# Kernel tuning notes

Hardware: AMD Instinct MI355X
Metric: run time of the kernel (lower is better)

Reference implementation:

```python
import jax, jax.numpy as jnp
import numpy as np

IMG = 32            # feature-map side == image_size
B, HC = 8, 3        # batch, hint channels
C, NH, L = 256, 8, 8  # model_channels, nhead, num_encoder_layers
DFF = 1025
HIN = IMG * 8       # hint resolution (three stride-2 convs => /8)
NEIGH = (7, 7)
CONV_SHAPES = [(16, HC), (16, 16), (32, 16), (32, 32), (96, 32), (96, 96), (256, 96), (C, 256)]
STRIDES = [1, 1, 2, 1, 2, 1, 2, 1]


def setup_inputs() -> dict:
    key = jax.random.key(0)
    ks = jax.random.split(key, 32)
    inp = {"hint": jax.random.normal(ks[0], (B, HC, HIN, HIN), jnp.float32)}
    for i, (co, ci) in enumerate(CONV_SHAPES):
        inp[f"conv_w{i}"] = jax.random.normal(ks[1 + i], (co, ci, 3, 3), jnp.float32) * 0.05
    base = 9
    def p(shape, j):
        return jax.random.normal(ks[base + j], (L,) + shape, jnp.float32) * 0.02
    inp["in_proj_w"] = p((3 * C, C), 0)
    inp["in_proj_b"] = p((3 * C,), 1)
    inp["out_w"] = p((C, C), 2)
    inp["out_b"] = p((C,), 3)
    inp["lin1_w"] = p((DFF, C), 4)
    inp["lin1_b"] = p((DFF,), 5)
    inp["lin2_w"] = p((C, DFF), 6)
    inp["lin2_b"] = p((C,), 7)
    inp["ln1_w"] = jnp.ones((L, C), jnp.float32)
    inp["ln1_b"] = jnp.zeros((L, C), jnp.float32)
    inp["ln2_w"] = jnp.ones((L, C), jnp.float32)
    inp["ln2_b"] = jnp.zeros((L, C), jnp.float32)
    return inp


def _conv(x, w, s):
    # torch Conv2d(k=3, padding=1, stride=s, bias=False)
    return jax.lax.conv_general_dilated(x, w, (s, s), [(1, 1), (1, 1)],
                                        dimension_numbers=("NCHW", "OIHW", "NCHW"))


def _sine_pos(h, w, c):
    # DETR/UniAD PositionEmbeddingSine (normalize=False, temperature=1e4) -> (h*w, c)
    npf = c // 2
    y = jnp.broadcast_to(jnp.arange(1, h + 1, dtype=jnp.float32)[:, None], (h, w))
    x = jnp.broadcast_to(jnp.arange(1, w + 1, dtype=jnp.float32)[None, :], (h, w))
    dim_t = 10000.0 ** (2.0 * (jnp.arange(npf, dtype=jnp.float32) // 2) / npf)
    px = x[..., None] / dim_t
    py = y[..., None] / dim_t
    px = jnp.stack([jnp.sin(px[..., 0::2]), jnp.cos(px[..., 1::2])], -1).reshape(h, w, npf)
    py = jnp.stack([jnp.sin(py[..., 0::2]), jnp.cos(py[..., 1::2])], -1).reshape(h, w, npf)
    return jnp.concatenate([py, px], -1).reshape(h * w, c)


def _neigh_mask(h, w, hm, wm):
    # vectorized version of generate_mask: 0 inside the hm x wm neighborhood, -inf outside
    ih = jnp.arange(h)
    iw = jnp.arange(w)
    dh = jnp.abs(ih[:, None] - ih[None, :]) <= hm // 2   # (h, h)
    dw = jnp.abs(iw[:, None] - iw[None, :]) <= wm // 2   # (w, w)
    allowed = (dh[:, None, :, None] & dw[None, :, None, :]).reshape(h * w, h * w)
    return jnp.where(allowed, 0.0, -1e9).astype(jnp.float32)


def _ln(x, g, b):
    mu = x.mean(-1, keepdims=True)
    v = ((x - mu) ** 2).mean(-1, keepdims=True)
    return (x - mu) / jnp.sqrt(v + 1e-5) * g + b


def _forward(hint, conv_ws, params):
    x = hint
    for i, (w, s) in enumerate(zip(conv_ws, STRIDES)):
        x = _conv(x, w, s)
        if i < len(conv_ws) - 1:
            x = jax.nn.silu(x)
    b, c, h, w = x.shape
    src = x.reshape(b, c, h * w).transpose(0, 2, 1)          # (B, N, C), N h-major
    pos = _sine_pos(h, w, c)[None]                           # (1, N, C)
    mask = _neigh_mask(h, w, *NEIGH)                         # (N, N)
    dh = c // NH
    scale = 1.0 / np.sqrt(dh).astype(np.float32)

    def layer(s, p):
        ipw, ipb, ow, ob, l1w, l1b, l2w, l2b, g1, b1, g2, b2 = p
        qk_in = s + pos
        q = (qk_in @ ipw[:c].T + ipb[:c]).reshape(b, -1, NH, dh)
        k = (qk_in @ ipw[c:2 * c].T + ipb[c:2 * c]).reshape(b, -1, NH, dh)
        v = (s @ ipw[2 * c:].T + ipb[2 * c:]).reshape(b, -1, NH, dh)
        sc = jnp.einsum('bnhd,bmhd->bhnm', q, k) * scale + mask
        a = jax.nn.softmax(sc, -1)
        ctx = jnp.einsum('bhnm,bmhd->bnhd', a, v).reshape(b, -1, c)
        s = _ln(s + ctx @ ow.T + ob, g1, b1)                 # post-norm
        ff = jax.nn.relu(s @ l1w.T + l1b) @ l2w.T + l2b      # dropout inactive (eval)
        return _ln(s + ff, g2, b2), None

    src, _ = jax.lax.scan(layer, src, params)
    return src.transpose(0, 2, 1).reshape(b, c, h, w)        # '(h w) b c -> b c h w'


def reference(hint, conv_w0, conv_w1, conv_w2, conv_w3, conv_w4, conv_w5, conv_w6, conv_w7,
              in_proj_w, in_proj_b, out_w, out_b, lin1_w, lin1_b, lin2_w, lin2_b,
              ln1_w, ln1_b, ln2_w, ln2_b):
    conv_ws = (conv_w0, conv_w1, conv_w2, conv_w3, conv_w4, conv_w5, conv_w6, conv_w7)
    params = (in_proj_w, in_proj_b, out_w, out_b, lin1_w, lin1_b, lin2_w, lin2_b,
              ln1_w, ln1_b, ln2_w, ln2_b)
    return _forward(hint, conv_ws, params)
```

## Files before the change

### kernel.cpp

```cpp
#include <hip/hip_runtime.h>
#include <hip/hip_bf16.h>


typedef __bf16 bf16x8 __attribute__((ext_vector_type(8)));
typedef float f32x4 __attribute__((ext_vector_type(4)));
typedef unsigned short us8v __attribute__((ext_vector_type(8)));

__device__ __forceinline__ unsigned short f2bf(float f) {
  unsigned int u = __float_as_uint(f);
  unsigned int r = (u + 0x7fffu + ((u >> 16) & 1u)) >> 16;
  return (unsigned short)r;
}
__device__ __forceinline__ float bf2f(unsigned short h) {
  return __uint_as_float(((unsigned int)h) << 16);
}

#define GLD16(src, dst)                                                        \
  __builtin_amdgcn_global_load_lds(                                            \
      (const __attribute__((address_space(1))) unsigned int*)(src),            \
      (__attribute__((address_space(3))) unsigned int*)(dst), 16, 0, 0)

template<int BM, int BN, int NT, int MODE, int LNF = 0, int KTC = 0>
__global__ __launch_bounds__(NT) void k_gemm(
    const unsigned short* __restrict__ A, int lda,
    const unsigned short* __restrict__ Bw, int ldb,
    const float* __restrict__ bias, const float* __restrict__ posadd,
    float* __restrict__ C, unsigned short* __restrict__ Cb, int ldc,
    int K, int Nstore, int act, int omode, long long zsB, long long zsC,
    const unsigned short* __restrict__ zpage, int Ci, int Hi, int stride, int lw,
    int divm, int divs, const float* __restrict__ lng, const float* __restrict__ lnb)
{
  constexpr int NW = NT / 64;
  constexpr int NWN = (NT == 512) ? 4 : ((BN >= 128) ? 2 : 1);
  constexpr int NWM = NW / NWN;
  constexpr int WM = BM / NWM, WN = BN / NWN;
  constexpr int MF = WM / 16, NF = WN / 16;
  constexpr int AIS = (BM * 8) / NT;
  constexpr int BIS = (BN * 8) / NT;
  __shared__ unsigned short lA[2][BM * 64];
  __shared__ unsigned short lB[2][BN * 64];
  __shared__ float red[2][32][2];
  int tid = threadIdx.x, lane = tid & 63, wid = tid >> 6;
  int bm = blockIdx.x * BM, bn = blockIdx.y * BN;
  const unsigned short* Bz = Bw + (size_t)blockIdx.z * zsB;

  int j = (lane & 7) ^ (lane >> 3);
  int e8 = (j & 3) << 3;
  int halfl = j >> 2;

  size_t arow[AIS], brow[BIS];
  int hb[AIS], wb[AIS];
  size_t ab[AIS];
#pragma unroll
  for (int i = 0; i < AIS; ++i) {
    int rr = (wid + i * NW) * 8 + (lane >> 3);
    if constexpr (MODE == 0) {
      arow[i] = (size_t)(bm + rr) * lda + (j << 3);
    } else {
      int pos = bm + rr;
      int b = pos >> (2 * lw);
      int rem = pos & ((1 << (2 * lw)) - 1);
      int ho = rem >> lw, wo = rem & ((1 << lw) - 1);
      hb[i] = ho * stride - 1;
      wb[i] = wo * stride - 1;
      ab[i] = (size_t)b * Hi * Hi * Ci;
    }
  }
#pragma unroll
  for (int i = 0; i < BIS; ++i)
    brow[i] = (size_t)(bn + (wid + i * NW) * 8 + (lane >> 3)) * ldb + (j << 3);

  auto stage = [&](int buf, int kt) {
    if constexpr (MODE == 1) {
      int s0 = kt * 2, s1 = s0 + 1;
      int t0 = (s0 * divm) >> divs, t1 = (s1 * divm) >> divs;
      int cipw = Ci >> 5;
      int cc0 = (s0 - t0 * cipw) << 5, cc1 = (s1 - t1 * cipw) << 5;
      int kh0 = (t0 * 171) >> 9, kw0 = t0 - kh0 * 3;
      int kh1 = (t1 * 171) >> 9, kw1 = t1 - kh1 * 3;
      int kh = halfl ? kh1 : kh0;
      int kw = halfl ? kw1 : kw0;
      int cco = halfl ? cc1 : cc0;
      bool tv = (halfl ? t1 : t0) < 9;
#pragma unroll
      for (int i = 0; i < AIS; ++i) {
        int hi = hb[i] + kh, wi = wb[i] + kw;
        const unsigned short* ap =
            (tv && (unsigned)hi < (unsigned)Hi && (unsigned)wi < (unsigned)Hi)
                ? (A + ab[i] + (size_t)(hi * Hi + wi) * Ci + cco + e8)
                : zpage;
        GLD16(ap, &lA[buf][(wid + i * NW) * 512]);
      }
    } else {
#pragma unroll
      for (int i = 0; i < AIS; ++i)
        GLD16(A + arow[i] + kt * 64, &lA[buf][(wid + i * NW) * 512]);
    }
#pragma unroll
    for (int i = 0; i < BIS; ++i)
      GLD16(Bz + brow[i] + kt * 64, &lB[buf][(wid + i * NW) * 512]);
  };

  f32x4 acc[MF][NF];
#pragma unroll
  for (int m = 0; m < MF; ++m)
#pragma unroll
    for (int n = 0; n < NF; ++n)
#pragma unroll
      for (int q = 0; q < 4; ++q) acc[m][n][q] = 0.f;

  int wn = wid % NWN, wm = wid / NWN;
  int r0 = wm * WM + (lane & 15);
  int c0 = wn * WN + (lane & 15);
  int sl0 = (((lane >> 4)) ^ (lane & 7)) << 3;
  int sl1 = (((lane >> 4) + 4) ^ (lane & 7)) << 3;
  const int nkt = (KTC > 0) ? KTC : (K >> 6);
  int cur = 0;
  stage(0, 0);
#pragma unroll
  for (int kt = 0; kt < nkt; ++kt) {
    if (kt + 1 < nkt) {
      stage(cur ^ 1, kt + 1);
      asm volatile("s_waitcnt vmcnt(%0)" : : "n"(AIS + BIS) : "memory");
    } else {
      asm volatile("s_waitcnt vmcnt(0)" : : : "memory");
    }
    __builtin_amdgcn_s_barrier();
    asm volatile("" ::: "memory");
    bf16x8 a0[MF], a1[MF], b0[NF], b1[NF];
#pragma unroll
    for (int m = 0; m < MF; ++m) {
      a0[m] = *(const bf16x8*)&lA[cur][(r0 + m * 16) * 64 + sl0];
      a1[m] = *(const bf16x8*)&lA[cur][(r0 + m * 16) * 64 + sl1];
    }
#pragma unroll
    for (int n = 0; n < NF; ++n) {
      b0[n] = *(const bf16x8*)&lB[cur][(c0 + n * 16) * 64 + sl0];
      b1[n] = *(const bf16x8*)&lB[cur][(c0 + n * 16) * 64 + sl1];
    }
#pragma unroll
    for (int m = 0; m < MF; ++m)
#pragma unroll
      for (int n = 0; n < NF; ++n)
        acc[m][n] = __builtin_amdgcn_mfma_f32_16x16x32_bf16(a0[m], b0[n], acc[m][n], 0, 0, 0);
#pragma unroll
    for (int m = 0; m < MF; ++m)
#pragma unroll
      for (int n = 0; n < NF; ++n)
        acc[m][n] = __builtin_amdgcn_mfma_f32_16x16x32_bf16(a1[m], b1[n], acc[m][n], 0, 0, 0);
    asm volatile("" ::: "memory");
    __builtin_amdgcn_s_barrier();
    cur ^= 1;
  }

  int colb = bn + wn * WN + (lane & 15);
  int rowb = bm + wm * WM + ((lane >> 4) << 2);

  if constexpr (LNF) {
    float x[NF][4];
    float sums[4] = {0.f, 0.f, 0.f, 0.f}, sqs[4] = {0.f, 0.f, 0.f, 0.f};
#pragma unroll
    for (int n = 0; n < NF; ++n) {
      int col = colb + n * 16;
      float bs = bias[col];
#pragma unroll
      for (int q = 0; q < 4; ++q) {
        int row = rowb + q;
        float v = acc[0][n][q] + bs + C[(size_t)row * 256 + col];
        x[n][q] = v;
        sums[q] += v;
        sqs[q] += v * v;
      }
    }
#pragma unroll
    for (int q = 0; q < 4; ++q) {
      sums[q] += __shfl_xor(sums[q], 1); sqs[q] += __shfl_xor(sqs[q], 1);
      sums[q] += __shfl_xor(sums[q], 2); sqs[q] += __shfl_xor(sqs[q], 2);
      sums[q] += __shfl_xor(sums[q], 4); sqs[q] += __shfl_xor(sqs[q], 4);
      sums[q] += __shfl_xor(sums[q], 8); sqs[q] += __shfl_xor(sqs[q], 8);
    }
    int rl = wm * 16 + ((lane >> 4) << 2);
    if ((lane & 15) == 0) {
#pragma unroll
      for (int q = 0; q < 4; ++q) {
        red[wn][rl + q][0] = sums[q];
        red[wn][rl + q][1] = sqs[q];
      }
    }
    __syncthreads();
#pragma unroll
    for (int q = 0; q < 4; ++q) {
      float ts = sums[q] + red[wn ^ 1][rl + q][0];
      float tq = sqs[q] + red[wn ^ 1][rl + q][1];
      float mu = ts * (1.f / 256.f);
      float var = tq * (1.f / 256.f) - mu * mu;
      float rs = rsqrtf(var + 1e-5f);
      int row = rowb + q;
#pragma unroll
      for (int n = 0; n < NF; ++n) {
        int col = colb + n * 16;
        float o = (x[n][q] - mu) * rs * lng[col] + lnb[col];
        C[(size_t)row * 256 + col] = o;
        Cb[(size_t)row * 256 + col] = f2bf(o);
      }
    }
    return;
  }

  float* Cz = C ? C + (size_t)blockIdx.z * zsC : nullptr;
  unsigned short* Cbz = Cb ? Cb + (size_t)blockIdx.z * zsC : nullptr;
#pragma unroll
  for (int n = 0; n < NF; ++n) {
    int col = colb + n * 16;
    if (col >= Nstore) continue;
    float bs = bias ? bias[col] : 0.f;
#pragma unroll
    for (int m = 0; m < MF; ++m) {
#pragma unroll
      for (int q = 0; q < 4; ++q) {
        int row = rowb + m * 16 + q;
        float v = acc[m][n][q] + bs;
        if (posadd && col < 512) v += posadd[((row & 1023) << 9) + col];
        if (act == 1) v = fmaxf(v, 0.f);
        else if (act == 2) v = v / (1.f + __expf(-v));
        size_t off = (size_t)row * ldc + col;
        if (omode == 0) Cz[off] = v;
        else if (omode == 1) Cbz[off] = f2bf(v);
        else { Cz[off] = v; Cbz[off] = f2bf(v); }
      }
    }
  }
}

template<int S>
__global__ __launch_bounds__(256) void k_conv_direct(
    const unsigned short* __restrict__ x, const unsigned short* __restrict__ wp,
    int ldw, unsigned short* __restrict__ y, int Hi, int Ho, int Wo, int lwt)
{
  constexpr int HR = 7 * S + 3;
  constexpr int HC = 15 * S + 3;
  constexpr int HP = HR * HC;
  __shared__ unsigned short xs[HP * 40];
  __shared__ unsigned short wsh[32 * 312];
  int tid = threadIdx.x, lane = tid & 63, wv = tid >> 6;
  int b = blockIdx.y;
  int tr = blockIdx.x >> lwt, tc = blockIdx.x & ((1 << lwt) - 1);
  int hi0 = tr * 8 * S - 1, wi0 = tc * 16 * S - 1;

  for (int u = tid; u < HP * 8; u += 256) {
    int pix = u >> 3, part = u & 7;
    int hr = pix / HC, hcc = pix - hr * HC;
    int hi = hi0 + hr, wi = wi0 + hcc;
    ushort4 v = {0, 0, 0, 0};
    if ((unsigned)hi < (unsigned)Hi && (unsigned)wi < (unsigned)Hi)
      v = *(const ushort4*)(x + ((size_t)(b * Hi + hi) * Hi + wi) * 32 + part * 4);
    *(ushort4*)(&xs[pix * 40 + part * 4]) = v;
  }
  for (int u = tid; u < 2304; u += 256) {
    int co = u / 72, kk = (u - co * 72) * 4;
    *(ushort4*)(&wsh[co * 312 + kk]) = *(const ushort4*)(wp + (size_t)co * ldw + kk);
  }
  __syncthreads();

  int cL = lane & 15, kq = (lane >> 4) << 3;
  f32x4 acc[2][2];
#pragma unroll
  for (int m = 0; m < 2; ++m)
#pragma unroll
    for (int n = 0; n < 2; ++n)
#pragma unroll
      for (int q = 0; q < 4; ++q) acc[m][n][q] = 0.f;

#pragma unroll
  for (int tap = 0; tap < 9; ++tap) {
    const int kh = tap / 3, kw = tap % 3;
    bf16x8 af[2], bfr[2];
#pragma unroll
    for (int m = 0; m < 2; ++m) {
      int hr = (wv * 2 + m) * S + kh;
      int hc = cL * S + kw;
      af[m] = *(const bf16x8*)&xs[(hr * HC + hc) * 40 + kq];
    }
#pragma unroll
    for (int n = 0; n < 2; ++n)
      bfr[n] = *(const bf16x8*)&wsh[(cL + n * 16) * 312 + tap * 32 + kq];
#pragma unroll
    for (int m = 0; m < 2; ++m)
#pragma unroll
      for (int n = 0; n < 2; ++n)
        acc[m][n] = __builtin_amdgcn_mfma_f32_16x16x32_bf16(af[m], bfr[n], acc[m][n], 0, 0, 0);
  }

  int wo0 = tc * 16 + ((lane >> 4) << 2);
#pragma unroll
  for (int m = 0; m < 2; ++m) {
    int ho = tr * 8 + wv * 2 + m;
#pragma unroll
    for (int n = 0; n < 2; ++n) {
      int co = cL + n * 16;
#pragma unroll
      for (int q = 0; q < 4; ++q) {
        float v = acc[m][n][q];
        v = v / (1.f + __expf(-v));
        y[((size_t)(b * Ho + ho) * Wo + wo0 + q) * 32 + co] = f2bf(v);
      }
    }
  }
}

__global__ __launch_bounds__(256) void k_im2col0(
    const float* __restrict__ x, unsigned short* __restrict__ dst, int row0, int total)
{
  for (int idx = blockIdx.x * 256 + threadIdx.x; idx < total; idx += gridDim.x * 256) {
    int r = idx >> 6, e = idx & 63;
    int pos = row0 + r;
    int b = pos >> 16, rem = pos & 65535, ho = rem >> 8, wo = rem & 255;
    unsigned short val = 0;
    if (e < 27) {
      int t9 = e / 3, ci = e - t9 * 3;
      int hi = ho + (t9 / 3) - 1, wi = wo + (t9 - (t9 / 3) * 3) - 1;
      if ((unsigned)hi < 256u && (unsigned)wi < 256u)
        val = f2bf(x[(((size_t)b * 3 + ci) << 16) + (hi << 8) + wi]);
    }
    dst[idx] = val;
  }
}

__global__ __launch_bounds__(256) void k_wperm(
    const float* __restrict__ w, unsigned short* __restrict__ wp,
    int Co, int CiR, int CiP, int CoP, int Kpad)
{
  int idx = blockIdx.x * 256 + threadIdx.x;
  if (idx >= CoP * Kpad) return;
  int co = idx / Kpad, k = idx - co * Kpad;
  int t = k / CiP, ci = k - t * CiP;
  float v = 0.f;
  if (co < Co && t < 9 && ci < CiR) v = w[((size_t)co * CiR + ci) * 9 + t];
  wp[idx] = f2bf(v);
}

__global__ void k_cvt_pad(const float* __restrict__ in, unsigned short* __restrict__ outb,
                          float* __restrict__ outf, int R, int C, int Rp, int Cp)
{
  int l = blockIdx.y;
  int total = Rp * Cp;
  for (int idx = blockIdx.x * 256 + threadIdx.x; idx < total; idx += gridDim.x * 256) {
    int r = idx / Cp, c = idx - r * Cp;
    float v = (r < R && c < C) ? in[((size_t)l * R + r) * C + c] : 0.f;
    size_t o = (size_t)l * total + idx;
    if (outb) outb[o] = f2bf(v);
    if (outf) outf[o] = v;
  }
}

__global__ __launch_bounds__(256) void k_pos(unsigned short* __restrict__ posb)
{
  int n = blockIdx.x, c = threadIdx.x;
  int ih = n >> 5, iw = n & 31;
  float coord = (c < 128) ? (float)(ih + 1) : (float)(iw + 1);
  int cc = c & 127;
  float e = (float)((cc >> 1) << 1) * (1.f / 128.f);
  float t = coord / powf(10000.f, e);
  posb[(n << 8) + c] = f2bf((cc & 1) ? cosf(t) : sinf(t));
}

__global__ __launch_bounds__(256) void k_attn(
    const unsigned short* __restrict__ qkv, unsigned short* __restrict__ ctx)
{
  __shared__ float k_lds[196 * 36];
  __shared__ unsigned short v_lds[848 * 8];
  __shared__ float p_lds[64 * 50];
  int bx = blockIdx.x;
  int b = bx >> 4, tile = bx & 15;
  int th8 = ((tile >> 2) << 3), tw8 = ((tile & 3) << 3);
  int g = blockIdx.y;
  int tid = threadIdx.x, lane = tid & 63, wid = tid >> 6;
  int h0e = max(th8 - 3, 0), h1e = min(th8 + 10, 31);
  int w0e = max(tw8 - 3, 0), w1e = min(tw8 + 10, 31);
  int nh = h1e - h0e + 1, nw = w1e - w0e + 1;
  int nkeys = nh * nw, nslots = nkeys * 4;
  unsigned int magic = (65536u + (unsigned)nw - 1u) / (unsigned)nw;
  size_t qbase = (size_t)((unsigned)b << 10) * 768;

  for (int s = tid; s < 784; s += 256) {
    int sc = min(s, nslots - 1);
    int uidx = sc >> 2, oct = sc & 3;
    int hh = (int)(((unsigned)uidx * magic) >> 16);
    int ww = uidx - hh * nw;
    hh += h0e; ww += w0e;
    const unsigned short* kp = qkv + qbase + (size_t)((hh << 5) + ww) * 768 + 256 + (g << 5) + oct * 8;
    us8v u = *(const us8v*)kp;
    float* dst = &k_lds[uidx * 36 + oct * 8];
    f32x4 w0, w1;
#pragma unroll
    for (int q = 0; q < 4; ++q) { w0[q] = bf2f(u[q]); w1[q] = bf2f(u[q + 4]); }
    *(f32x4*)dst = w0;
    *(f32x4*)(dst + 4) = w1;
  }
#pragma unroll
  for (int i = 0; i < 4; ++i) {
    int base = i * 256 + wid * 64;
    if (base < 784) {
      int s = min(base + lane, nslots - 1);
      int uidx = s >> 2, chunk = s & 3;
      int hh = (int)(((unsigned)uidx * magic) >> 16);
      int ww = uidx - hh * nw;
      hh += h0e; ww += w0e;
      const unsigned short* vp = qkv + qbase + (size_t)((hh << 5) + ww) * 768 + 512 + (g << 5) + chunk * 8;
      GLD16(vp, &v_lds[base * 8]);
    }
  }
  __syncthreads();

  int q = tid >> 2, dq = tid & 3;
  int qh = th8 + (q >> 3), qw = tw8 + (q & 7);
  const float scale = 0.17677669529663687f;
  const unsigned short* qp = qkv + qbase + (size_t)((qh << 5) + qw) * 768 + (g << 5) + dq * 8;
  us8v uq = *(const us8v*)qp;
  float qr[8];
#pragma unroll
  for (int t = 0; t < 8; ++t) qr[t] = bf2f(uq[t]) * scale;

  int rbase[7], cofs[7];
  bool rval[7], cval[7];
#pragma unroll
  for (int d = 0; d < 7; ++d) {
    int mh = qh - 3 + d;
    rval[d] = (unsigned)mh < 32u;
    rbase[d] = (mh - h0e) * nw;
    int mw = qw - 3 + d;
    cval[d] = (unsigned)mw < 32u;
    cofs[d] = mw - w0e;
  }

  float m = -1e30f;
#pragma unroll
  for (int kk = 0; kk < 49; ++kk) {
    const int d7 = kk / 7, r7 = kk % 7;
    bool valid = rval[d7] && cval[r7];
    int uidx = valid ? (rbase[d7] + cofs[r7]) : 0;
    const float* kr = &k_lds[uidx * 36 + dq * 8];
    f32x4 a0 = *(const f32x4*)kr, a1 = *(const f32x4*)(kr + 4);
    float d = 0.f;
#pragma unroll
    for (int t = 0; t < 4; ++t) d = fmaf(qr[t], a0[t], d);
#pragma unroll
    for (int t = 0; t < 4; ++t) d = fmaf(qr[4 + t], a1[t], d);
    d += __shfl_xor(d, 1);
    d += __shfl_xor(d, 2);
    float s_kk = valid ? d : -1e30f;
    m = fmaxf(m, s_kk);
    if (dq == (kk & 3)) p_lds[q * 50 + kk] = s_kk;
  }
  float sum = 0.f;
  for (int kk = dq; kk < 49; kk += 4) {
    float e = __expf(p_lds[q * 50 + kk] - m);
    p_lds[q * 50 + kk] = e;
    sum += e;
  }
  sum += __shfl_xor(sum, 1);
  sum += __shfl_xor(sum, 2);
  float inv = 1.f / sum;

  float acc[8] = {};
#pragma unroll
  for (int kk = 0; kk < 49; ++kk) {
    const int d7 = kk / 7, r7 = kk % 7;
    int uidx = (rval[d7] && cval[r7]) ? (rbase[d7] + cofs[r7]) : 0;
    float pb = p_lds[q * 50 + kk];
    us8v uv = *(const us8v*)&v_lds[uidx * 32 + dq * 8];
#pragma unroll
    for (int t = 0; t < 8; ++t) acc[t] = fmaf(pb, bf2f(uv[t]), acc[t]);
  }
  unsigned short* op = ctx + ((size_t)((b << 10) + (qh << 5) + qw) << 8) + (g << 5) + dq * 8;
  us8v out;
#pragma unroll
  for (int t = 0; t < 8; ++t) out[t] = f2bf(acc[t] * inv);
  *(us8v*)op = out;
}

__global__ void k_nxc_to_cxn(const float* __restrict__ x, float* __restrict__ y)
{
  __shared__ float t[32][33];
  int b = blockIdx.z;
  int c0 = blockIdx.x * 32, n0 = blockIdx.y * 32;
  int tx = threadIdx.x, ty = threadIdx.y;
  t[ty][tx] = x[((size_t)(b * 1024 + n0 + ty)) * 256 + c0 + tx];
  __syncthreads();
  y[((size_t)(b * 256 + c0 + ty)) * 1024 + n0 + tx] = t[tx][ty];
}

extern "C" void kernel_launch(void* const* d_in, const int* in_sizes, int n_in,
                              void* d_out, int out_size, void* d_ws, size_t ws_size,
                              hipStream_t stream)
{
  const float* hint = (const float*)d_in[0];
  const float* cw[8];
  for (int i = 0; i < 8; ++i) cw[i] = (const float*)d_in[1 + i];
  const float* ipw  = (const float*)d_in[9];
  const float* ipb  = (const float*)d_in[10];
  const float* outw = (const float*)d_in[11];
  const float* outb = (const float*)d_in[12];
  const float* l1w  = (const float*)d_in[13];
  const float* l1b  = (const float*)d_in[14];
  const float* l2w  = (const float*)d_in[15];
  const float* l2b  = (const float*)d_in[16];
  const float* g1   = (const float*)d_in[17];
  const float* b1   = (const float*)d_in[18];
  const float* g2   = (const float*)d_in[19];
  const float* b2   = (const float*)d_in[20];

  float* ws = (float*)d_ws;
  size_t off = 0;
  float* bufA = ws + off; off += 8388608;
  float* bufB = ws + off; off += 8388608;
  float* src  = ws + off; off += 2097152;
  unsigned short* srcb = (unsigned short*)(ws + off); off += 1048576;
  unsigned short* posb = (unsigned short*)(ws + off); off += 131072;
  float* posqk = ws + off; off += 4194304;
  unsigned short* wqkvb = (unsigned short*)(ws + off); off += 786432;
  unsigned short* outwb = (unsigned short*)(ws + off); off += 262144;
  unsigned short* l1wb  = (unsigned short*)(ws + off); off += 1179648;
  unsigned short* l2wb  = (unsigned short*)(ws + off); off += 1179648;
  float* l1bp = ws + off; off += 9216;
  unsigned short* cwp[8];
  const int CoPs[8]  = {128, 32, 32, 32, 128, 128, 256, 256};
  const int CiRs[8]  = {3, 16, 16, 32, 32, 96, 96, 256};
  const int CiPs[8]  = {3, 32, 32, 32, 32, 96, 96, 256};
  const int Kpads[8] = {64, 288, 288, 288, 320, 896, 896, 2304};
  const int Cos[8]   = {16, 16, 32, 32, 96, 96, 256, 256};
  for (int i = 0; i < 8; ++i) { cwp[i] = (unsigned short*)(ws + off); off += ((size_t)CoPs[i] * Kpads[i] + 1) / 2; }
  unsigned short* zpage = (unsigned short*)(ws + off); off += 64;

  hipMemsetAsync(zpage, 0, 256, stream);

  k_cvt_pad<<<dim3(768, 8), 256, 0, stream>>>(ipw,  wqkvb, nullptr, 768, 256, 768, 256);
  k_cvt_pad<<<dim3(256, 8), 256, 0, stream>>>(outw, outwb, nullptr, 256, 256, 256, 256);
  k_cvt_pad<<<dim3(1152, 8), 256, 0, stream>>>(l1w, l1wb, nullptr, 1025, 256, 1152, 256);
  k_cvt_pad<<<dim3(1152, 8), 256, 0, stream>>>(l2w, l2wb, nullptr, 256, 1025, 256, 1152);
  k_cvt_pad<<<dim3(5, 8), 256, 0, stream>>>(l1b, nullptr, l1bp, 1025, 1, 1152, 1);
  for (int i = 0; i < 8; ++i)
    k_wperm<<<(CoPs[i] * Kpads[i] + 255) / 256, 256, 0, stream>>>(
        cw[i], cwp[i], Cos[i], CiRs[i], CiPs[i], CoPs[i], Kpads[i]);
  k_pos<<<dim3(1024), 256, 0, stream>>>(posb);

  unsigned short* bufAu = (unsigned short*)bufA;
  unsigned short* bufBu = (unsigned short*)bufB;
  unsigned short* imbu  = (unsigned short*)bufB;

#define GEMM_TAIL nullptr, 0, 0, 0, 0, 0, 0, nullptr, nullptr
  for (int c = 0; c < 4; ++c) {
    k_im2col0<<<8192, 256, 0, stream>>>(hint, imbu, c * 131072, 131072 * 64);
    k_gemm<128, 32, 256, 0, 0, 1><<<dim3(1024, 1), 256, 0, stream>>>(
        imbu, 64, cwp[0], 64, nullptr, nullptr, nullptr,
        bufAu + (size_t)c * 131072 * 32, 32, 64, 32, 2, 1, 0, 0, GEMM_TAIL);
  }
  k_conv_direct<1><<<dim3(512, 8), 256, 0, stream>>>(bufAu, cwp[1], 288, bufBu, 256, 256, 256, 4);
  k_conv_direct<2><<<dim3(128, 8), 256, 0, stream>>>(bufBu, cwp[2], 288, bufAu, 256, 128, 128, 3);
  k_conv_direct<1><<<dim3(128, 8), 256, 0, stream>>>(bufAu, cwp[3], 288, bufBu, 128, 128, 128, 3);
  k_gemm<128, 128, 512, 1, 0, 5><<<dim3(256, 1), 512, 0, stream>>>(
      bufBu, 0, cwp[4], 320, nullptr, nullptr, nullptr, bufAu, 96, 320, 96, 2, 1,
      0, 0, zpage, 32, 128, 2, 6, 1, 0, nullptr, nullptr);
  k_gemm<128, 128, 512, 1, 0, 14><<<dim3(256, 1), 512, 0, stream>>>(
      bufAu, 0, cwp[5], 896, nullptr, nullptr, nullptr, bufBu, 96, 896, 96, 2, 1,
      0, 0, zpage, 96, 64, 1, 6, 171, 9, nullptr, nullptr);
  k_gemm<64, 128, 512, 1, 0, 14><<<dim3(128, 2), 512, 0, stream>>>(
      bufBu, 0, cwp[6], 896, nullptr, nullptr, nullptr, bufAu, 256, 896, 256, 2, 1,
      0, 0, zpage, 96, 64, 2, 5, 171, 9, nullptr, nullptr);
  k_gemm<64, 128, 512, 1><<<dim3(128, 2), 512, 0, stream>>>(
      bufAu, 0, cwp[7], 2304, nullptr, nullptr, src, srcb, 256, 2304, 256, 0, 2,
      0, 0, zpage, 256, 32, 1, 5, 1, 3, nullptr, nullptr);

  k_gemm<64, 128, 512, 0, 0, 4><<<dim3(16, 4, 8), 512, 0, stream>>>(
      posb, 256, wqkvb, 256, nullptr, nullptr, posqk, nullptr, 512, 256, 512, 0, 0,
      196608LL, 524288LL, GEMM_TAIL);

  unsigned short* qkvb = bufAu;
  unsigned short* ctx  = (unsigned short*)(bufA + 3145728);
  unsigned short* ff   = (unsigned short*)(bufB + 2097152);

  for (int l = 0; l < 8; ++l) {
    const unsigned short* wqkv_l = wqkvb + (size_t)l * 768 * 256;
    const float* ipb_l  = ipb  + (size_t)l * 768;
    const unsigned short* outw_l = outwb + (size_t)l * 256 * 256;
    const float* outb_l = outb + (size_t)l * 256;
    const unsigned short* l1w_l = l1wb + (size_t)l * 1152 * 256;
    const float* l1b_l  = l1bp + (size_t)l * 1152;
    const unsigned short* l2w_l = l2wb + (size_t)l * 256 * 1152;
    const float* l2b_l  = l2b  + (size_t)l * 256;
    const float* posqk_l = posqk + (size_t)l * 524288;
    const float* g1_l = g1 + l * 256; const float* b1_l = b1 + l * 256;
    const float* g2_l = g2 + l * 256; const float* b2_l = b2 + l * 256;

    k_gemm<64, 128, 512, 0, 0, 4><<<dim3(128, 6), 512, 0, stream>>>(
        srcb, 256, wqkv_l, 256, ipb_l, posqk_l, nullptr, qkvb, 768, 256, 768, 0, 1,
        0, 0, GEMM_TAIL);
    k_attn<<<dim3(128, 8), 256, 0, stream>>>(qkvb, ctx);
    k_gemm<32, 256, 256, 0, 1, 4><<<dim3(256, 1), 256, 0, stream>>>(
        ctx, 256, outw_l, 256, outb_l, nullptr, src, srcb, 256, 256, 256, 0, 0,
        0, 0, nullptr, 0, 0, 0, 0, 0, 0, g1_l, b1_l);
    k_gemm<64, 128, 512, 0, 0, 4><<<dim3(128, 9), 512, 0, stream>>>(
        srcb, 256, l1w_l, 256, l1b_l, nullptr, nullptr, ff, 1152, 256, 1152, 1, 1,
        0, 0, GEMM_TAIL);
    k_gemm<32, 256, 256, 0, 1><<<dim3(256, 1), 256, 0, stream>>>(
        ff, 1152, l2w_l, 1152, l2b_l, nullptr, src, srcb, 256, 1152, 256, 0, 0,
        0, 0, nullptr, 0, 0, 0, 0, 0, 0, g2_l, b2_l);
  }

  k_nxc_to_cxn<<<dim3(8, 32, 8), dim3(32, 32), 0, stream>>>(src, (float*)d_out);
}
```

Before: 994.4 us.

## Fuse first conv into direct kernel, batch weight perms, bf16 K in attention

Replaces the im2col plus GEMM path for the first 3-channel conv with a direct fp32 kernel. It writes SiLU outputs straight into the padded 32-channel bf16 layout, which removes four im2col passes and their intermediate buffer. The eight weight-permute launches become one batched kernel, with conv0 weights now read directly. In attention, K is kept as bf16 in LDS and loaded asynchronously alongside V instead of being converted to fp32 through registers. The FFN2 GEMM also gets a compile-time K-tile count. The risks are lower arithmetic efficiency for the scalar conv0 and extra bf16 unpacking inside the attention inner loop.

```diff
diff --git a/kernel.cpp b/kernel.cpp
--- a/kernel.cpp
+++ b/kernel.cpp
@@ -232,6 +232,56 @@
   }
 }
 
+__global__ __launch_bounds__(256) void k_conv0(
+    const float* __restrict__ x, const float* __restrict__ w,
+    unsigned short* __restrict__ y)
+{
+  __shared__ float ws[16][28];
+  int tid = threadIdx.x;
+  for (int u = tid; u < 432; u += 256) {
+    int co = u / 27, k = u - co * 27;
+    int t = k / 3, ci = k - t * 3;
+    ws[co][k] = w[((size_t)co * 3 + ci) * 9 + t];
+  }
+  __syncthreads();
+  int h = blockIdx.x, b = blockIdx.y, wo = tid;
+  float xin[3][3][3];
+#pragma unroll
+  for (int ci = 0; ci < 3; ++ci)
+#pragma unroll
+    for (int kh = 0; kh < 3; ++kh) {
+      int hi = h + kh - 1;
+#pragma unroll
+      for (int kw = 0; kw < 3; ++kw) {
+        int wi = wo + kw - 1;
+        xin[ci][kh][kw] = ((unsigned)hi < 256u && (unsigned)wi < 256u)
+            ? x[(((size_t)b * 3 + ci) << 16) + (hi << 8) + wi] : 0.f;
+      }
+    }
+  float acc[16] = {};
+#pragma unroll
+  for (int t = 0; t < 9; ++t) {
+    const int kh = t / 3, kw = t % 3;
+#pragma unroll
+    for (int ci = 0; ci < 3; ++ci) {
+      float xv = xin[ci][kh][kw];
+#pragma unroll
+      for (int co = 0; co < 16; ++co)
+        acc[co] = fmaf(xv, ws[co][t * 3 + ci], acc[co]);
+    }
+  }
+  us8v o0, o1, zv;
+#pragma unroll
+  for (int q = 0; q < 8; ++q) {
+    float v0 = acc[q];     v0 = v0 / (1.f + __expf(-v0)); o0[q] = f2bf(v0);
+    float v1 = acc[q + 8]; v1 = v1 / (1.f + __expf(-v1)); o1[q] = f2bf(v1);
+    zv[q] = 0;
+  }
+  unsigned short* yp = y + ((((size_t)b << 16) + (h << 8) + wo) << 5);
+  *(us8v*)(yp) = o0; *(us8v*)(yp + 8) = o1;
+  *(us8v*)(yp + 16) = zv; *(us8v*)(yp + 24) = zv;
+}
+
 template<int S>
 __global__ __launch_bounds__(256) void k_conv_direct(
     const unsigned short* __restrict__ x, const unsigned short* __restrict__ wp,
@@ -308,35 +358,26 @@
   }
 }
 
-__global__ __launch_bounds__(256) void k_im2col0(
-    const float* __restrict__ x, unsigned short* __restrict__ dst, int row0, int total)
-{
+struct WP8 { const float* w[8]; unsigned short* q[8]; };
+__global__ __launch_bounds__(256) void k_wperm_all(WP8 p)
+{
+  const int CoPs[8]  = {128, 32, 32, 32, 128, 128, 256, 256};
+  const int CiRs[8]  = {3, 16, 16, 32, 32, 96, 96, 256};
+  const int CiPs[8]  = {3, 32, 32, 32, 32, 96, 96, 256};
+  const int Kpads[8] = {64, 288, 288, 288, 320, 896, 896, 2304};
+  const int Cos[8]   = {16, 16, 32, 32, 96, 96, 256, 256};
+  int i = blockIdx.y + 1;
+  const float* w = p.w[i];
+  unsigned short* wp = p.q[i];
+  int Kpad = Kpads[i], CiP = CiPs[i], CiR = CiRs[i], Co = Cos[i];
+  int total = CoPs[i] * Kpad;
   for (int idx = blockIdx.x * 256 + threadIdx.x; idx < total; idx += gridDim.x * 256) {
-    int r = idx >> 6, e = idx & 63;
-    int pos = row0 + r;
-    int b = pos >> 16, rem = pos & 65535, ho = rem >> 8, wo = rem & 255;
-    unsigned short val = 0;
-    if (e < 27) {
-      int t9 = e / 3, ci = e - t9 * 3;
-      int hi = ho + (t9 / 3) - 1, wi = wo + (t9 - (t9 / 3) * 3) - 1;
-      if ((unsigned)hi < 256u && (unsigned)wi < 256u)
-        val = f2bf(x[(((size_t)b * 3 + ci) << 16) + (hi << 8) + wi]);
-    }
-    dst[idx] = val;
-  }
-}
-
-__global__ __launch_bounds__(256) void k_wperm(
-    const float* __restrict__ w, unsigned short* __restrict__ wp,
-    int Co, int CiR, int CiP, int CoP, int Kpad)
-{
-  int idx = blockIdx.x * 256 + threadIdx.x;
-  if (idx >= CoP * Kpad) return;
-  int co = idx / Kpad, k = idx - co * Kpad;
-  int t = k / CiP, ci = k - t * CiP;
-  float v = 0.f;
-  if (co < Co && t < 9 && ci < CiR) v = w[((size_t)co * CiR + ci) * 9 + t];
-  wp[idx] = f2bf(v);
+    int co = idx / Kpad, k = idx - co * Kpad;
+    int t = k / CiP, ci = k - t * CiP;
+    float v = 0.f;
+    if (co < Co && t < 9 && ci < CiR) v = w[((size_t)co * CiR + ci) * 9 + t];
+    wp[idx] = f2bf(v);
+  }
 }
 
 __global__ void k_cvt_pad(const float* __restrict__ in, unsigned short* __restrict__ outb,
@@ -367,7 +408,7 @@
 __global__ __launch_bounds__(256) void k_attn(
     const unsigned short* __restrict__ qkv, unsigned short* __restrict__ ctx)
 {
-  __shared__ float k_lds[196 * 36];
+  __shared__ unsigned short k_ldsu[848 * 8];
   __shared__ unsigned short v_lds[848 * 8];
   __shared__ float p_lds[64 * 50];
   int bx = blockIdx.x;
@@ -382,21 +423,6 @@
   unsigned int magic = (65536u + (unsigned)nw - 1u) / (unsigned)nw;
   size_t qbase = (size_t)((unsigned)b << 10) * 768;
 
-  for (int s = tid; s < 784; s += 256) {
-    int sc = min(s, nslots - 1);
-    int uidx = sc >> 2, oct = sc & 3;
-    int hh = (int)(((unsigned)uidx * magic) >> 16);
-    int ww = uidx - hh * nw;
-    hh += h0e; ww += w0e;
-    const unsigned short* kp = qkv + qbase + (size_t)((hh << 5) + ww) * 768 + 256 + (g << 5) + oct * 8;
-    us8v u = *(const us8v*)kp;
-    float* dst = &k_lds[uidx * 36 + oct * 8];
-    f32x4 w0, w1;
-#pragma unroll
-    for (int q = 0; q < 4; ++q) { w0[q] = bf2f(u[q]); w1[q] = bf2f(u[q + 4]); }
-    *(f32x4*)dst = w0;
-    *(f32x4*)(dst + 4) = w1;
-  }
 #pragma unroll
   for (int i = 0; i < 4; ++i) {
     int base = i * 256 + wid * 64;
@@ -406,8 +432,9 @@
       int hh = (int)(((unsigned)uidx * magic) >> 16);
       int ww = uidx - hh * nw;
       hh += h0e; ww += w0e;
-      const unsigned short* vp = qkv + qbase + (size_t)((hh << 5) + ww) * 768 + 512 + (g << 5) + chunk * 8;
-      GLD16(vp, &v_lds[base * 8]);
+      const unsigned short* rp = qkv + qbase + (size_t)((hh << 5) + ww) * 768 + (g << 5) + chunk * 8;
+      GLD16(rp + 256, &k_ldsu[base * 8]);
+      GLD16(rp + 512, &v_lds[base * 8]);
     }
   }
   __syncthreads();
@@ -439,13 +466,10 @@
     const int d7 = kk / 7, r7 = kk % 7;
     bool valid = rval[d7] && cval[r7];
     int uidx = valid ? (rbase[d7] + cofs[r7]) : 0;
-    const float* kr = &k_lds[uidx * 36 + dq * 8];
-    f32x4 a0 = *(const f32x4*)kr, a1 = *(const f32x4*)(kr + 4);
+    us8v uk = *(const us8v*)&k_ldsu[uidx * 32 + dq * 8];
     float d = 0.f;
 #pragma unroll
-    for (int t = 0; t < 4; ++t) d = fmaf(qr[t], a0[t], d);
-#pragma unroll
-    for (int t = 0; t < 4; ++t) d = fmaf(qr[4 + t], a1[t], d);
+    for (int t = 0; t < 8; ++t) d = fmaf(qr[t], bf2f(uk[t]), d);
     d += __shfl_xor(d, 1);
     d += __shfl_xor(d, 2);
     float s_kk = valid ? d : -1e30f;
@@ -525,10 +549,7 @@
   float* l1bp = ws + off; off += 9216;
   unsigned short* cwp[8];
   const int CoPs[8]  = {128, 32, 32, 32, 128, 128, 256, 256};
-  const int CiRs[8]  = {3, 16, 16, 32, 32, 96, 96, 256};
-  const int CiPs[8]  = {3, 32, 32, 32, 32, 96, 96, 256};
   const int Kpads[8] = {64, 288, 288, 288, 320, 896, 896, 2304};
-  const int Cos[8]   = {16, 16, 32, 32, 96, 96, 256, 256};
   for (int i = 0; i < 8; ++i) { cwp[i] = (unsigned short*)(ws + off); off += ((size_t)CoPs[i] * Kpads[i] + 1) / 2; }
   unsigned short* zpage = (unsigned short*)(ws + off); off += 64;
 
@@ -539,22 +560,16 @@
   k_cvt_pad<<<dim3(1152, 8), 256, 0, stream>>>(l1w, l1wb, nullptr, 1025, 256, 1152, 256);
   k_cvt_pad<<<dim3(1152, 8), 256, 0, stream>>>(l2w, l2wb, nullptr, 256, 1025, 256, 1152);
   k_cvt_pad<<<dim3(5, 8), 256, 0, stream>>>(l1b, nullptr, l1bp, 1025, 1, 1152, 1);
-  for (int i = 0; i < 8; ++i)
-    k_wperm<<<(CoPs[i] * Kpads[i] + 255) / 256, 256, 0, stream>>>(
-        cw[i], cwp[i], Cos[i], CiRs[i], CiPs[i], CoPs[i], Kpads[i]);
+  WP8 wpargs;
+  for (int i = 0; i < 8; ++i) { wpargs.w[i] = cw[i]; wpargs.q[i] = cwp[i]; }
+  k_wperm_all<<<dim3(64, 7), 256, 0, stream>>>(wpargs);
   k_pos<<<dim3(1024), 256, 0, stream>>>(posb);
 
   unsigned short* bufAu = (unsigned short*)bufA;
   unsigned short* bufBu = (unsigned short*)bufB;
-  unsigned short* imbu  = (unsigned short*)bufB;
 
 #define GEMM_TAIL nullptr, 0, 0, 0, 0, 0, 0, nullptr, nullptr
-  for (int c = 0; c < 4; ++c) {
-    k_im2col0<<<8192, 256, 0, stream>>>(hint, imbu, c * 131072, 131072 * 64);
-    k_gemm<128, 32, 256, 0, 0, 1><<<dim3(1024, 1), 256, 0, stream>>>(
-        imbu, 64, cwp[0], 64, nullptr, nullptr, nullptr,
-        bufAu + (size_t)c * 131072 * 32, 32, 64, 32, 2, 1, 0, 0, GEMM_TAIL);
-  }
+  k_conv0<<<dim3(256, 8), 256, 0, stream>>>(hint, cw[0], bufAu);
   k_conv_direct<1><<<dim3(512, 8), 256, 0, stream>>>(bufAu, cwp[1], 288, bufBu, 256, 256, 256, 4);
   k_conv_direct<2><<<dim3(128, 8), 256, 0, stream>>>(bufBu, cwp[2], 288, bufAu, 256, 128, 128, 3);
   k_conv_direct<1><<<dim3(128, 8), 256, 0, stream>>>(bufAu, cwp[3], 288, bufBu, 128, 128, 128, 3);
@@ -602,7 +617,7 @@
     k_gemm<64, 128, 512, 0, 0, 4><<<dim3(128, 9), 512, 0, stream>>>(
         srcb, 256, l1w_l, 256, l1b_l, nullptr, nullptr, ff, 1152, 256, 1152, 1, 1,
         0, 0, GEMM_TAIL);
-    k_gemm<32, 256, 256, 0, 1><<<dim3(256, 1), 256, 0, stream>>>(
+    k_gemm<32, 256, 256, 0, 1, 18><<<dim3(256, 1), 256, 0, stream>>>(
         ff, 1152, l2w_l, 1152, l2b_l, nullptr, src, srcb, 256, 1152, 256, 0, 0,
         0, 0, nullptr, 0, 0, 0, 0, 0, 0, g2_l, b2_l);
   }
```

Measured after the change: 911.9 us. -8.3%, faster.
